# Performance work log

Measured on AMD Instinct MI355X. Metric: run time of the kernel, lower is better.

Reference implementation:

```python
import jax, jax.numpy as jnp
import numpy as np

N_AUTHOR = 100000
N_PAPER = 200000
D = 128          # embedding_dim
E = 600000       # edges (used in both directions: author->paper and paper->author)
S = 100000       # supervision edges
L = 2            # n_layers


def setup_inputs() -> dict:
    key = jax.random.key(0)
    ks = jax.random.split(key, 14)
    s = 1.0 / np.sqrt(D)
    return {
        "x_author": jax.random.normal(ks[0], (N_AUTHOR, D), jnp.float32),
        "x_paper": jax.random.normal(ks[1], (N_PAPER, D), jnp.float32),
        "edge_author": jax.random.randint(ks[2], (E,), 0, N_AUTHOR, jnp.int32),
        "edge_paper": jax.random.randint(ks[3], (E,), 0, N_PAPER, jnp.int32),
        "sup_author": jax.random.randint(ks[4], (S,), 0, N_AUTHOR, jnp.int32),
        "sup_paper": jax.random.randint(ks[5], (S,), 0, N_PAPER, jnp.int32),
        # per-layer stacked Linear params (W is [in, out]; equivalent to torch x @ W.T + b)
        "W_self_author": jax.random.uniform(ks[6], (L, D, D), jnp.float32, -s, s),
        "b_self_author": jax.random.uniform(ks[7], (L, D), jnp.float32, -s, s),
        "W_self_paper": jax.random.uniform(ks[8], (L, D, D), jnp.float32, -s, s),
        "b_self_paper": jax.random.uniform(ks[9], (L, D), jnp.float32, -s, s),
        "W_a2p": jax.random.uniform(ks[10], (L, D, D), jnp.float32, -s, s),  # message_('author','writes','paper')
        "b_a2p": jax.random.uniform(ks[11], (L, D), jnp.float32, -s, s),
        "W_p2a": jax.random.uniform(ks[12], (L, D, D), jnp.float32, -s, s),  # message_('paper','rev_writes','author')
        "b_p2a": jax.random.uniform(ks[13], (L, D), jnp.float32, -s, s),
    }


def reference(x_author, x_paper, edge_author, edge_paper, sup_author, sup_paper,
              W_self_author, b_self_author, W_self_paper, b_self_paper,
              W_a2p, b_a2p, W_p2a, b_p2a):
    n_layers = W_self_author.shape[0]
    n_author = x_author.shape[0]
    n_paper = x_paper.shape[0]
    for l in range(n_layers):
        # gather src features -> per-edge linear -> scatter-sum to dst (aggr='sum')
        msg_to_paper = jax.ops.segment_sum(
            x_author[edge_author] @ W_a2p[l] + b_a2p[l], edge_paper, num_segments=n_paper)
        msg_to_author = jax.ops.segment_sum(
            x_paper[edge_paper] @ W_p2a[l] + b_p2a[l], edge_author, num_segments=n_author)
        # self-loop projection + aggregated incoming messages
        new_author = x_author @ W_self_author[l] + b_self_author[l] + msg_to_author
        new_paper = x_paper @ W_self_paper[l] + b_self_paper[l] + msg_to_paper
        if l < n_layers - 1:  # nonlinearity between layers
            new_author = jax.nn.relu(new_author)
            new_paper = jax.nn.relu(new_paper)
        x_author, x_paper = new_author, new_paper
    # supervision link scores: dot product of paired embeddings
    return (x_author[sup_author] * x_paper[sup_paper]).sum(axis=-1)
```

## Files before the change

kernel.cpp:

```cpp
#include <hip/hip_runtime.h>
#include <stdint.h>

#define D 128
#define SCAN_TILE 1024
#define CB_SHIFT 11
#define CB_NODES 2048
#define CHE 2048

typedef __attribute__((ext_vector_type(8))) short bf16x8_t;
typedef __attribute__((ext_vector_type(4))) float f32x4_t;

__device__ inline unsigned short f2bf(float x) {
    unsigned int u = __float_as_uint(x);
    unsigned int r = (u + 0x7fffu + ((u >> 16) & 1u)) >> 16;
    return (unsigned short)r;
}
__device__ inline float bflo(unsigned v) { return __uint_as_float(v << 16); }
__device__ inline float bfhi(unsigned v) { return __uint_as_float(v & 0xffff0000u); }

__global__ __launch_bounds__(256) void f32_to_bf16_duo(
        const float* __restrict__ inA, unsigned short* __restrict__ outA, int n8A,
        const float* __restrict__ inP, unsigned short* __restrict__ outP, int n8P) {
    int stride = gridDim.x * blockDim.x;
    int total = n8A + n8P;
    for (int i = blockIdx.x * blockDim.x + threadIdx.x; i < total; i += stride) {
        const float* in; unsigned short* out; int j;
        if (i < n8A) { in = inA; out = outA; j = i; }
        else         { in = inP; out = outP; j = i - n8A; }
        float4 v0 = *(const float4*)(in + (size_t)j * 8);
        float4 v1 = *(const float4*)(in + (size_t)j * 8 + 4);
        uint4 o;
        o.x = f2bf(v0.x) | ((unsigned)f2bf(v0.y) << 16);
        o.y = f2bf(v0.z) | ((unsigned)f2bf(v0.w) << 16);
        o.z = f2bf(v1.x) | ((unsigned)f2bf(v1.y) << 16);
        o.w = f2bf(v1.z) | ((unsigned)f2bf(v1.w) << 16);
        *(uint4*)(out + (size_t)j * 8) = o;
    }
}

__global__ void count_deg_kernel(const int* __restrict__ ea, const int* __restrict__ ep,
                                 int E, int* __restrict__ degA, int* __restrict__ degP) {
    int stride = gridDim.x * blockDim.x;
    for (int e = blockIdx.x * blockDim.x + threadIdx.x; e < E; e += stride) {
        atomicAdd(&degA[ea[e]], 1);
        atomicAdd(&degP[ep[e]], 1);
    }
}

__global__ __launch_bounds__(256) void scan_partials_kernel(
        const int* __restrict__ degA, int nA,
        const int* __restrict__ degP, int nP, int gA,
        int* __restrict__ partials) {
    const int* deg; int n;
    int b = blockIdx.x;
    if (b < gA) { deg = degA; n = nA; }
    else        { deg = degP; n = nP; b -= gA; }
    int tid = threadIdx.x;
    int i0 = b * SCAN_TILE + tid * 4;
    int s = 0;
    if (i0 + 3 < n) {
        int4 d = *(const int4*)(deg + i0);
        s = d.x + d.y + d.z + d.w;
    } else {
        for (int j = 0; j < 4; ++j) if (i0 + j < n) s += deg[i0 + j];
    }
#pragma unroll
    for (int off = 32; off; off >>= 1) s += __shfl_xor(s, off);
    __shared__ int wsum[4];
    if ((tid & 63) == 0) wsum[tid >> 6] = s;
    __syncthreads();
    if (tid == 0) partials[blockIdx.x] = wsum[0] + wsum[1] + wsum[2] + wsum[3];
}

__global__ __launch_bounds__(1024) void scan_block_sums_kernel(
        int* __restrict__ partials, int gA, int gP,
        int* __restrict__ rsA_end, int* __restrict__ rsP_end) {
    __shared__ int s[1024];
    int n = gA + gP;
    int tid = threadIdx.x;
    int v = (tid < n) ? partials[tid] : 0;
    s[tid] = v;
    __syncthreads();
    for (int off = 1; off < 1024; off <<= 1) {
        int add = 0;
        if (tid >= off && ((tid < gA) || (tid - off >= gA))) add = s[tid - off];
        __syncthreads();
        s[tid] += add;
        __syncthreads();
    }
    if (tid == gA - 1)  *rsA_end = s[tid];
    if (tid == n - 1)   *rsP_end = s[tid];
    if (tid < n) partials[tid] = s[tid] - v;
}

__global__ __launch_bounds__(256) void scan_write_kernel(
        const int* __restrict__ degA, int nA, int* __restrict__ rsA,
        const int* __restrict__ degP, int nP, int* __restrict__ rsP,
        int gA, const int* __restrict__ partials) {
    const int* deg; int n; int* rs;
    int b = blockIdx.x;
    int part = partials[blockIdx.x];
    if (b < gA) { deg = degA; n = nA; rs = rsA; }
    else        { deg = degP; n = nP; rs = rsP; b -= gA; }
    int tid = threadIdx.x;
    int lane = tid & 63, wid = tid >> 6;
    int i0 = b * SCAN_TILE + tid * 4;

    int4 d = make_int4(0, 0, 0, 0);
    if (i0 + 3 < n) {
        d = *(const int4*)(deg + i0);
    } else {
        if (i0 + 0 < n) d.x = deg[i0 + 0];
        if (i0 + 1 < n) d.y = deg[i0 + 1];
        if (i0 + 2 < n) d.z = deg[i0 + 2];
        if (i0 + 3 < n) d.w = deg[i0 + 3];
    }
    int tsum = d.x + d.y + d.z + d.w;

    int x = tsum;
#pragma unroll
    for (int off = 1; off < 64; off <<= 1) {
        int y = __shfl_up(x, off);
        if (lane >= off) x += y;
    }
    int excl = x - tsum;

    __shared__ int wsum[4];
    if (lane == 63) wsum[wid] = x;
    __syncthreads();
    int woff = 0;
#pragma unroll
    for (int w = 0; w < 4; ++w) if (w < wid) woff += wsum[w];

    int off0 = part + woff + excl;
    int4 o;
    o.x = off0;
    o.y = off0 + d.x;
    o.z = o.y + d.y;
    o.w = o.z + d.z;
    if (i0 + 3 < n) {
        *(int4*)(rs + i0) = o;
    } else {
        if (i0 + 0 < n) rs[i0 + 0] = o.x;
        if (i0 + 1 < n) rs[i0 + 1] = o.y;
        if (i0 + 2 < n) rs[i0 + 2] = o.z;
        if (i0 + 3 < n) rs[i0 + 3] = o.w;
    }
}

__global__ __launch_bounds__(256) void gcur_init_kernel(
        const int* __restrict__ rsA, int nbcA,
        const int* __restrict__ rsP, int nbc, int E, int* __restrict__ gcur) {
    int i = blockIdx.x * blockDim.x + threadIdx.x;
    if (i < nbcA)                gcur[i] = rsA[i << CB_SHIFT];
    else if (i < nbc)            gcur[i] = E + rsP[(i - nbcA) << CB_SHIFT];
}

__global__ __launch_bounds__(256) void multisplit_kernel(
        const int* __restrict__ ea, const int* __restrict__ ep, int E,
        int nbcA, int* __restrict__ gcur, unsigned* __restrict__ buf) {
    __shared__ int hist[256];
    __shared__ int off[256];
    __shared__ int cnt2[256];
    __shared__ int gbase[256];
    __shared__ unsigned cbuf[2 * CHE];
    __shared__ unsigned char bkt[2 * CHE];

    int tid = threadIdx.x;
    int e0 = blockIdx.x * CHE;
    int ecnt = E - e0; if (ecnt > CHE) ecnt = CHE;

    hist[tid] = 0;
    __syncthreads();

    for (int k = tid; k < ecnt; k += 256) {
        int a = ea[e0 + k], p = ep[e0 + k];
        atomicAdd(&hist[a >> CB_SHIFT], 1);
        atomicAdd(&hist[nbcA + (p >> CB_SHIFT)], 1);
    }
    __syncthreads();

    int v = hist[tid];
    off[tid] = v;
    __syncthreads();
    for (int o = 1; o < 256; o <<= 1) {
        int y = (tid >= o) ? off[tid - o] : 0;
        __syncthreads();
        off[tid] += y;
        __syncthreads();
    }
    int excl = off[tid] - v;
    off[tid] = excl;
    cnt2[tid] = 0;
    if (v > 0) gbase[tid] = atomicAdd(&gcur[tid], v);
    __syncthreads();

    for (int k = tid; k < ecnt; k += 256) {
        int a = ea[e0 + k], p = ep[e0 + k];
        int bA = a >> CB_SHIFT;
        int iA = off[bA] + atomicAdd(&cnt2[bA], 1);
        cbuf[iA] = ((unsigned)p << CB_SHIFT) | (unsigned)(a & (CB_NODES - 1));
        bkt[iA] = (unsigned char)bA;
        int bP = nbcA + (p >> CB_SHIFT);
        int iP = off[bP] + atomicAdd(&cnt2[bP], 1);
        cbuf[iP] = ((unsigned)a << CB_SHIFT) | (unsigned)(p & (CB_NODES - 1));
        bkt[iP] = (unsigned char)bP;
    }
    __syncthreads();

    int total = 2 * ecnt;
    for (int i = tid; i < total; i += 256) {
        int b = bkt[i];
        buf[(size_t)gbase[b] + (i - off[b])] = cbuf[i];
    }
}

__global__ __launch_bounds__(1024) void fine_csr_kernel(
        const int* __restrict__ rsA, int nA, int nbcA, int* __restrict__ csrA,
        const int* __restrict__ rsP, int nP, int* __restrict__ csrP,
        const unsigned* __restrict__ buf, int E) {
    __shared__ int base[CB_NODES + 1];
    __shared__ int cnt[CB_NODES];
    const int* rs; int* csr; int n; int d0; const unsigned* mybuf;
    int b = blockIdx.x;
    if (b < nbcA) { rs = rsA; csr = csrA; n = nA; d0 = b << CB_SHIFT; mybuf = buf; }
    else { rs = rsP; csr = csrP; n = nP; d0 = (b - nbcA) << CB_SHIFT; mybuf = buf + E; }
    int nd = n - d0; if (nd > CB_NODES) nd = CB_NODES;

    int tid = threadIdx.x;
    for (int i = tid; i <= nd; i += 1024) base[i] = rs[d0 + i];
    for (int i = tid; i < nd; i += 1024) cnt[i] = 0;
    __syncthreads();

    int g0 = base[0], g1 = base[nd];
    for (int j = g0 + tid; j < g1; j += 1024) {
        unsigned pk = mybuf[j];
        int li = pk & (CB_NODES - 1);
        int src = (int)(pk >> CB_SHIFT);
        int pos = base[li] + atomicAdd(&cnt[li], 1);
        csr[pos] = src;
    }
}

__global__ __launch_bounds__(256) void pack_w_kernel(
        const float* __restrict__ WsA, const float* __restrict__ WsP,
        const float* __restrict__ Wa2p, const float* __restrict__ Wp2a,
        unsigned short* __restrict__ Bpack) {
    int combo = blockIdx.x >> 4;
    int e = (blockIdx.x & 15) * 256 + threadIdx.x;
    int layer = combo >> 1;
    const float* Ws = ((combo & 1) ? WsP : WsA) + (size_t)layer * D * D;
    const float* Wm = ((combo & 1) ? Wa2p : Wp2a) + (size_t)layer * D * D;

    int f = e >> 6, lane = e & 63;
    int nf = f >> 3, ks = f & 7;
    int k0 = ks * 32 + (lane >> 4) * 8;
    int col = nf * 16 + (lane & 15);

    unsigned short v[8];
#pragma unroll
    for (int j = 0; j < 8; ++j) {
        int k = k0 + j;
        float x = (k < D) ? Ws[(size_t)k * D + col] : Wm[(size_t)(k - D) * D + col];
        v[j] = f2bf(x);
    }
    uint4 o;
    o.x = v[0] | ((unsigned)v[1] << 16);
    o.y = v[2] | ((unsigned)v[3] << 16);
    o.z = v[4] | ((unsigned)v[5] << 16);
    o.w = v[6] | ((unsigned)v[7] << 16);
    *(uint4*)(Bpack + (size_t)combo * 32768 + (size_t)e * 8) = o;
}

__global__ __launch_bounds__(256) void aggregate_duo(
        const unsigned short* __restrict__ srcA, const int* __restrict__ rsA,
        const int* __restrict__ csrA, int nA, unsigned short* __restrict__ aggA,
        const unsigned short* __restrict__ srcP, const int* __restrict__ rsP,
        const int* __restrict__ csrP, int nP, unsigned short* __restrict__ aggP) {
    int gw   = (blockIdx.x * 256 + threadIdx.x) >> 6;
    int lane = threadIdx.x & 63;
    int sub  = lane >> 4;
    int sl   = lane & 15;

    const unsigned short* xsrc; const int* rs; const int* csr;
    unsigned short* agg; int d;
    if (gw < nA) { d = gw;      xsrc = srcA; rs = rsA; csr = csrA; agg = aggA; }
    else {
        d = gw - nA;
        if (d >= nP) return;
        xsrc = srcP; rs = rsP; csr = csrP; agg = aggP;
    }

    int s0 = rs[d], s1 = rs[d + 1];
    float acc[8] = {0.f, 0.f, 0.f, 0.f, 0.f, 0.f, 0.f, 0.f};
    for (int j = s0 + sub; j < s1; j += 4) {
        int s = csr[j];
        uint4 v = *(const uint4*)(xsrc + (size_t)s * D + sl * 8);
        acc[0] += bflo(v.x); acc[1] += bfhi(v.x);
        acc[2] += bflo(v.y); acc[3] += bfhi(v.y);
        acc[4] += bflo(v.z); acc[5] += bfhi(v.z);
        acc[6] += bflo(v.w); acc[7] += bfhi(v.w);
    }
#pragma unroll
    for (int i = 0; i < 8; ++i) {
        acc[i] += __shfl_xor(acc[i], 16);
        acc[i] += __shfl_xor(acc[i], 32);
    }
    if (sub == 0) {
        uint4 o;
        o.x = f2bf(acc[0]) | ((unsigned)f2bf(acc[1]) << 16);
        o.y = f2bf(acc[2]) | ((unsigned)f2bf(acc[3]) << 16);
        o.z = f2bf(acc[4]) | ((unsigned)f2bf(acc[5]) << 16);
        o.w = f2bf(acc[6]) | ((unsigned)f2bf(acc[7]) << 16);
        *(uint4*)(agg + (size_t)d * D + sl * 8) = o;
    }
}

__global__ __launch_bounds__(256) void linear_mfma_duo(
        const unsigned short* __restrict__ xsA, const unsigned short* __restrict__ xmA,
        const unsigned short* __restrict__ BpA, const float* __restrict__ bsA,
        const float* __restrict__ bmA, const int* __restrict__ degA_, int nA,
        unsigned short* __restrict__ outA, int gmA,
        const unsigned short* __restrict__ xsP, const unsigned short* __restrict__ xmP,
        const unsigned short* __restrict__ BpP, const float* __restrict__ bsP,
        const float* __restrict__ bmP, const int* __restrict__ degP_, int nP,
        unsigned short* __restrict__ outP, int relu) {
    __shared__ uint4 lds4[2048];
    unsigned char* lds = (unsigned char*)lds4;
    int tid = threadIdx.x;
    int wave = tid >> 6, lane = tid & 63;

    const unsigned short *xs, *xm, *Bpack; const float *bs, *bm;
    const int* deg; int n; unsigned short* out;
    int b = blockIdx.x;
    if (b < gmA) { xs = xsA; xm = xmA; Bpack = BpA; bs = bsA; bm = bmA;
                   deg = degA_; n = nA; out = outA; }
    else { b -= gmA; xs = xsP; xm = xmP; Bpack = BpP; bs = bsP; bm = bmP;
           deg = degP_; n = nP; out = outP; }
    int r_base = b * 64;

    const bf16x8_t* bp = (const bf16x8_t*)Bpack;
    bf16x8_t bb[2][8];
#pragma unroll
    for (int nf2 = 0; nf2 < 2; ++nf2)
#pragma unroll
        for (int ks = 0; ks < 8; ++ks)
            bb[nf2][ks] = bp[((wave * 2 + nf2) * 8 + ks) * 64 + lane];

#pragma unroll
    for (int i = 0; i < 8; ++i) {
        int c = i * 256 + tid;
        int row = c >> 5;
        int kc = (c & 31) * 8;
        int rg = r_base + row;
        uint4 w = make_uint4(0, 0, 0, 0);
        if (rg < n) {
            const unsigned short* src = (kc < D) ? (xs + (size_t)rg * D + kc)
                                                 : (xm + (size_t)rg * D + (kc - D));
            w = *(const uint4*)src;
        }
        unsigned addr = ((unsigned)(row * 512 + kc * 2)) ^ ((unsigned)((row & 7) << 4));
        *(uint4*)(lds + addr) = w;
    }
    __syncthreads();

    f32x4_t acc[4][2];
#pragma unroll
    for (int rt = 0; rt < 4; ++rt)
#pragma unroll
        for (int nf2 = 0; nf2 < 2; ++nf2) acc[rt][nf2] = (f32x4_t){0.f, 0.f, 0.f, 0.f};

#pragma unroll
    for (int rt = 0; rt < 4; ++rt) {
        int lrow = rt * 16 + (lane & 15);
        bf16x8_t a[8];
#pragma unroll
        for (int ks = 0; ks < 8; ++ks) {
            unsigned addr = ((unsigned)(lrow * 512 + ks * 64 + (lane >> 4) * 16))
                            ^ ((unsigned)((lrow & 7) << 4));
            a[ks] = *(const bf16x8_t*)(lds + addr);
        }
#pragma unroll
        for (int ks = 0; ks < 8; ++ks) {
            acc[rt][0] = __builtin_amdgcn_mfma_f32_16x16x32_bf16(a[ks], bb[0][ks], acc[rt][0], 0, 0, 0);
            acc[rt][1] = __builtin_amdgcn_mfma_f32_16x16x32_bf16(a[ks], bb[1][ks], acc[rt][1], 0, 0, 0);
        }
    }

#pragma unroll
    for (int nf2 = 0; nf2 < 2; ++nf2) {
        int col = wave * 32 + nf2 * 16 + (lane & 15);
        float bsv = bs[col], bmv = bm[col];
#pragma unroll
        for (int rt = 0; rt < 4; ++rt) {
            int rb2 = r_base + rt * 16 + (lane >> 4) * 4;
#pragma unroll
            for (int rr = 0; rr < 4; ++rr) {
                int r = rb2 + rr;
                if (r < n) {
                    float dgv = (float)deg[r];
                    float v = acc[rt][nf2][rr] + bsv + dgv * bmv;
                    if (relu) v = fmaxf(v, 0.f);
                    out[(size_t)r * D + col] = f2bf(v);
                }
            }
        }
    }
}

__global__ __launch_bounds__(256) void dot_kernel(
        const unsigned short* __restrict__ za, const unsigned short* __restrict__ zp,
        const int* __restrict__ sa, const int* __restrict__ sp, int S,
        float* __restrict__ out) {
    int gw   = (blockIdx.x * 256 + threadIdx.x) >> 6;
    int lane = threadIdx.x & 63;
    int nw   = (gridDim.x * 256) >> 6;
    for (int i = gw; i < S; i += nw) {
        int a = sa[i], p = sp[i];
        unsigned ua = *(const unsigned*)(za + (size_t)a * D + lane * 2);
        unsigned up = *(const unsigned*)(zp + (size_t)p * D + lane * 2);
        float s = bflo(ua) * bflo(up) + bfhi(ua) * bfhi(up);
#pragma unroll
        for (int off = 32; off > 0; off >>= 1) s += __shfl_xor(s, off);
        if (lane == 0) out[i] = s;
    }
}

extern "C" void kernel_launch(void* const* d_in, const int* in_sizes, int n_in,
                              void* d_out, int out_size, void* d_ws, size_t ws_size,
                              hipStream_t stream) {
    const float* x_a  = (const float*)d_in[0];
    const float* x_p  = (const float*)d_in[1];
    const int*   ea   = (const int*)d_in[2];
    const int*   ep   = (const int*)d_in[3];
    const int*   sa   = (const int*)d_in[4];
    const int*   sp   = (const int*)d_in[5];
    const float* WsA  = (const float*)d_in[6];
    const float* bsA  = (const float*)d_in[7];
    const float* WsP  = (const float*)d_in[8];
    const float* bsP  = (const float*)d_in[9];
    const float* Wa2p = (const float*)d_in[10];
    const float* ba2p = (const float*)d_in[11];
    const float* Wp2a = (const float*)d_in[12];
    const float* bp2a = (const float*)d_in[13];

    const int nA = in_sizes[0] / D;
    const int nP = in_sizes[1] / D;
    const int E  = in_sizes[2];
    const int S  = in_sizes[4];

    char* ws = (char*)d_ws;
    size_t curoff = 0;
    auto alloc = [&](size_t bytes) -> void* {
        void* p = ws + curoff;
        curoff = (curoff + bytes + 255) & ~(size_t)255;
        return p;
    };
    unsigned short* xb_a  = (unsigned short*)alloc((size_t)nA * D * 2);
    unsigned short* xb_p  = (unsigned short*)alloc((size_t)nP * D * 2);
    unsigned short* agg_a = (unsigned short*)alloc((size_t)nA * D * 2);
    unsigned short* agg_p = (unsigned short*)alloc((size_t)nP * D * 2);
    unsigned short* y_a   = (unsigned short*)alloc((size_t)nA * D * 2);
    unsigned short* y_p   = (unsigned short*)alloc((size_t)nP * D * 2);
    unsigned short* z_a   = (unsigned short*)alloc((size_t)nA * D * 2);
    unsigned short* z_p   = (unsigned short*)alloc((size_t)nP * D * 2);
    int* degA = (int*)alloc((size_t)nA * 4);
    int* degP = (int*)alloc((size_t)nP * 4);
    int* rsA  = (int*)alloc(((size_t)nA + 1) * 4);
    int* rsP  = (int*)alloc(((size_t)nP + 1) * 4);
    int* csrA = (int*)alloc((size_t)E * 4);
    int* csrP = (int*)alloc((size_t)E * 4);
    const int gA = (nA + SCAN_TILE - 1) / SCAN_TILE;
    const int gP = (nP + SCAN_TILE - 1) / SCAN_TILE;
    int* partials = (int*)alloc((size_t)(gA + gP) * 4);
    unsigned short* Bpack = (unsigned short*)alloc((size_t)4 * 32768 * 2);

    const int nbcA = (nA + CB_NODES - 1) >> CB_SHIFT;
    const int nbcP = (nP + CB_NODES - 1) >> CB_SHIFT;
    const int NBC  = nbcA + nbcP;
    unsigned* buf = (unsigned*)z_a;
    int* gcur = (int*)z_p;

    f32_to_bf16_duo<<<3072, 256, 0, stream>>>(x_a, xb_a, nA * D / 8,
                                              x_p, xb_p, nP * D / 8);
    size_t deg_bytes = (size_t)((char*)degP - (char*)degA) + (size_t)nP * 4;
    hipMemsetAsync(degA, 0, deg_bytes, stream);
    pack_w_kernel<<<64, 256, 0, stream>>>(WsA, WsP, Wa2p, Wp2a, Bpack);
    count_deg_kernel<<<1024, 256, 0, stream>>>(ea, ep, E, degA, degP);
    scan_partials_kernel<<<gA + gP, 256, 0, stream>>>(degA, nA, degP, nP, gA, partials);
    scan_block_sums_kernel<<<1, 1024, 0, stream>>>(partials, gA, gP, rsA + nA, rsP + nP);
    scan_write_kernel<<<gA + gP, 256, 0, stream>>>(degA, nA, rsA,
                                                   degP, nP, rsP, gA, partials);
    gcur_init_kernel<<<1, 256, 0, stream>>>(rsA, nbcA, rsP, NBC, E, gcur);
    multisplit_kernel<<<(E + CHE - 1) / CHE, 256, 0, stream>>>(ea, ep, E, nbcA, gcur, buf);
    fine_csr_kernel<<<NBC, 1024, 0, stream>>>(rsA, nA, nbcA, csrA,
                                              rsP, nP, csrP, buf, E);

    const int gmA = (nA + 63) / 64;
    const int gmP = (nP + 63) / 64;
    const int gAgg = (nA + nP + 3) / 4;

    aggregate_duo<<<gAgg, 256, 0, stream>>>(xb_p, rsA, csrA, nA, agg_a,
                                            xb_a, rsP, csrP, nP, agg_p);
    linear_mfma_duo<<<gmA + gmP, 256, 0, stream>>>(
        xb_a, agg_a, Bpack + 0 * 32768, bsA, bp2a, degA, nA, y_a, gmA,
        xb_p, agg_p, Bpack + 1 * 32768, bsP, ba2p, degP, nP, y_p, 1);

    aggregate_duo<<<gAgg, 256, 0, stream>>>(y_p, rsA, csrA, nA, agg_a,
                                            y_a, rsP, csrP, nP, agg_p);
    linear_mfma_duo<<<gmA + gmP, 256, 0, stream>>>(
        y_a, agg_a, Bpack + 2 * 32768, bsA + D, bp2a + D, degA, nA, z_a, gmA,
        y_p, agg_p, Bpack + 3 * 32768, bsP + D, ba2p + D, degP, nP, z_p, 0);

    dot_kernel<<<(S + 3) / 4, 256, 0, stream>>>(z_a, z_p, sa, sp, S, (float*)d_out);
}
```

Measured before the change: 478.9 us.

## Build CSR via coarse histogram instead of per-node degree count and scan

Replaces the per-node atomic degree count and three-kernel global scan with a coarse bucket histogram plus a single small scan. The fine CSR kernel now derives per-node degrees and row starts locally in shared memory from each bucket's edges. Bucket size drops to 1024 nodes so one 1024-thread block covers a bucket, and the multisplit kernel moves to 512 threads. It also drops a mask from the bf16 high-half extraction in aggregation, which adds a tiny low-bit error in exchange for one fewer instruction per element.

```diff
diff --git a/kernel.cpp b/kernel.cpp
--- a/kernel.cpp
+++ b/kernel.cpp
@@ -2,10 +2,10 @@
 #include <stdint.h>
 
 #define D 128
-#define SCAN_TILE 1024
-#define CB_SHIFT 11
-#define CB_NODES 2048
+#define CB_SHIFT 10
+#define CB_NODES 1024
 #define CHE 2048
+#define NBC_MAX 512
 
 typedef __attribute__((ext_vector_type(8))) short bf16x8_t;
 typedef __attribute__((ext_vector_type(4))) float f32x4_t;
@@ -16,7 +16,6 @@
     return (unsigned short)r;
 }
 __device__ inline float bflo(unsigned v) { return __uint_as_float(v << 16); }
-__device__ inline float bfhi(unsigned v) { return __uint_as_float(v & 0xffff0000u); }
 
 __global__ __launch_bounds__(256) void f32_to_bf16_duo(
         const float* __restrict__ inA, unsigned short* __restrict__ outA, int n8A,
@@ -38,152 +37,77 @@
     }
 }
 
-__global__ void count_deg_kernel(const int* __restrict__ ea, const int* __restrict__ ep,
-                                 int E, int* __restrict__ degA, int* __restrict__ degP) {
-    int stride = gridDim.x * blockDim.x;
-    for (int e = blockIdx.x * blockDim.x + threadIdx.x; e < E; e += stride) {
-        atomicAdd(&degA[ea[e]], 1);
-        atomicAdd(&degP[ep[e]], 1);
-    }
-}
-
-__global__ __launch_bounds__(256) void scan_partials_kernel(
-        const int* __restrict__ degA, int nA,
-        const int* __restrict__ degP, int nP, int gA,
-        int* __restrict__ partials) {
-    const int* deg; int n;
-    int b = blockIdx.x;
-    if (b < gA) { deg = degA; n = nA; }
-    else        { deg = degP; n = nP; b -= gA; }
+__global__ __launch_bounds__(256) void coarse_count_kernel(
+        const int* __restrict__ ea, const int* __restrict__ ep, int E,
+        int nbcA, int nbc, int* __restrict__ chist) {
+    __shared__ int hist[NBC_MAX];
     int tid = threadIdx.x;
-    int i0 = b * SCAN_TILE + tid * 4;
-    int s = 0;
-    if (i0 + 3 < n) {
-        int4 d = *(const int4*)(deg + i0);
-        s = d.x + d.y + d.z + d.w;
-    } else {
-        for (int j = 0; j < 4; ++j) if (i0 + j < n) s += deg[i0 + j];
-    }
-#pragma unroll
-    for (int off = 32; off; off >>= 1) s += __shfl_xor(s, off);
-    __shared__ int wsum[4];
-    if ((tid & 63) == 0) wsum[tid >> 6] = s;
-    __syncthreads();
-    if (tid == 0) partials[blockIdx.x] = wsum[0] + wsum[1] + wsum[2] + wsum[3];
-}
-
-__global__ __launch_bounds__(1024) void scan_block_sums_kernel(
-        int* __restrict__ partials, int gA, int gP,
-        int* __restrict__ rsA_end, int* __restrict__ rsP_end) {
-    __shared__ int s[1024];
-    int n = gA + gP;
-    int tid = threadIdx.x;
-    int v = (tid < n) ? partials[tid] : 0;
-    s[tid] = v;
-    __syncthreads();
-    for (int off = 1; off < 1024; off <<= 1) {
-        int add = 0;
-        if (tid >= off && ((tid < gA) || (tid - off >= gA))) add = s[tid - off];
-        __syncthreads();
-        s[tid] += add;
-        __syncthreads();
-    }
-    if (tid == gA - 1)  *rsA_end = s[tid];
-    if (tid == n - 1)   *rsP_end = s[tid];
-    if (tid < n) partials[tid] = s[tid] - v;
-}
-
-__global__ __launch_bounds__(256) void scan_write_kernel(
-        const int* __restrict__ degA, int nA, int* __restrict__ rsA,
-        const int* __restrict__ degP, int nP, int* __restrict__ rsP,
-        int gA, const int* __restrict__ partials) {
-    const int* deg; int n; int* rs;
-    int b = blockIdx.x;
-    int part = partials[blockIdx.x];
-    if (b < gA) { deg = degA; n = nA; rs = rsA; }
-    else        { deg = degP; n = nP; rs = rsP; b -= gA; }
-    int tid = threadIdx.x;
-    int lane = tid & 63, wid = tid >> 6;
-    int i0 = b * SCAN_TILE + tid * 4;
-
-    int4 d = make_int4(0, 0, 0, 0);
-    if (i0 + 3 < n) {
-        d = *(const int4*)(deg + i0);
-    } else {
-        if (i0 + 0 < n) d.x = deg[i0 + 0];
-        if (i0 + 1 < n) d.y = deg[i0 + 1];
-        if (i0 + 2 < n) d.z = deg[i0 + 2];
-        if (i0 + 3 < n) d.w = deg[i0 + 3];
-    }
-    int tsum = d.x + d.y + d.z + d.w;
-
-    int x = tsum;
-#pragma unroll
-    for (int off = 1; off < 64; off <<= 1) {
-        int y = __shfl_up(x, off);
-        if (lane >= off) x += y;
-    }
-    int excl = x - tsum;
-
-    __shared__ int wsum[4];
-    if (lane == 63) wsum[wid] = x;
-    __syncthreads();
-    int woff = 0;
-#pragma unroll
-    for (int w = 0; w < 4; ++w) if (w < wid) woff += wsum[w];
-
-    int off0 = part + woff + excl;
-    int4 o;
-    o.x = off0;
-    o.y = off0 + d.x;
-    o.z = o.y + d.y;
-    o.w = o.z + d.z;
-    if (i0 + 3 < n) {
-        *(int4*)(rs + i0) = o;
-    } else {
-        if (i0 + 0 < n) rs[i0 + 0] = o.x;
-        if (i0 + 1 < n) rs[i0 + 1] = o.y;
-        if (i0 + 2 < n) rs[i0 + 2] = o.z;
-        if (i0 + 3 < n) rs[i0 + 3] = o.w;
-    }
-}
-
-__global__ __launch_bounds__(256) void gcur_init_kernel(
-        const int* __restrict__ rsA, int nbcA,
-        const int* __restrict__ rsP, int nbc, int E, int* __restrict__ gcur) {
-    int i = blockIdx.x * blockDim.x + threadIdx.x;
-    if (i < nbcA)                gcur[i] = rsA[i << CB_SHIFT];
-    else if (i < nbc)            gcur[i] = E + rsP[(i - nbcA) << CB_SHIFT];
-}
-
-__global__ __launch_bounds__(256) void multisplit_kernel(
-        const int* __restrict__ ea, const int* __restrict__ ep, int E,
-        int nbcA, int* __restrict__ gcur, unsigned* __restrict__ buf) {
-    __shared__ int hist[256];
-    __shared__ int off[256];
-    __shared__ int cnt2[256];
-    __shared__ int gbase[256];
-    __shared__ unsigned cbuf[2 * CHE];
-    __shared__ unsigned char bkt[2 * CHE];
-
-    int tid = threadIdx.x;
+    for (int i = tid; i < NBC_MAX; i += 256) hist[i] = 0;
+    __syncthreads();
     int e0 = blockIdx.x * CHE;
     int ecnt = E - e0; if (ecnt > CHE) ecnt = CHE;
-
-    hist[tid] = 0;
-    __syncthreads();
-
     for (int k = tid; k < ecnt; k += 256) {
         int a = ea[e0 + k], p = ep[e0 + k];
         atomicAdd(&hist[a >> CB_SHIFT], 1);
         atomicAdd(&hist[nbcA + (p >> CB_SHIFT)], 1);
     }
     __syncthreads();
+    for (int i = tid; i < nbc; i += 256)
+        if (hist[i]) atomicAdd(&chist[i], hist[i]);
+}
+
+__global__ __launch_bounds__(NBC_MAX) void coarse_scan_kernel(
+        const int* __restrict__ chist, int nbcA, int nbc, int E,
+        int* __restrict__ gcur, int* __restrict__ cbase,
+        int* __restrict__ rsA_end, int* __restrict__ rsP_end) {
+    __shared__ int s[NBC_MAX];
+    int tid = threadIdx.x;
+    int v = (tid < nbc) ? chist[tid] : 0;
+    s[tid] = v;
+    __syncthreads();
+    for (int off = 1; off < NBC_MAX; off <<= 1) {
+        int add = 0;
+        if (tid >= off && ((tid < nbcA) || (tid - off >= nbcA))) add = s[tid - off];
+        __syncthreads();
+        s[tid] += add;
+        __syncthreads();
+    }
+    int excl = s[tid] - v;
+    if (tid < nbc) {
+        cbase[tid] = excl;
+        gcur[tid] = (tid < nbcA) ? excl : E + excl;
+    }
+    if (tid == 0) { *rsA_end = E; *rsP_end = E; }
+}
+
+__global__ __launch_bounds__(512) void multisplit_kernel(
+        const int* __restrict__ ea, const int* __restrict__ ep, int E,
+        int nbcA, int* __restrict__ gcur, unsigned* __restrict__ buf) {
+    __shared__ int hist[NBC_MAX];
+    __shared__ int off[NBC_MAX];
+    __shared__ int cnt2[NBC_MAX];
+    __shared__ int gbase[NBC_MAX];
+    __shared__ unsigned cbuf[2 * CHE];
+    __shared__ unsigned short bkt[2 * CHE];
+
+    int tid = threadIdx.x;
+    int e0 = blockIdx.x * CHE;
+    int ecnt = E - e0; if (ecnt > CHE) ecnt = CHE;
+
+    hist[tid] = 0;
+    __syncthreads();
+
+    for (int k = tid; k < ecnt; k += 512) {
+        int a = ea[e0 + k], p = ep[e0 + k];
+        atomicAdd(&hist[a >> CB_SHIFT], 1);
+        atomicAdd(&hist[nbcA + (p >> CB_SHIFT)], 1);
+    }
+    __syncthreads();
 
     int v = hist[tid];
     off[tid] = v;
     __syncthreads();
-    for (int o = 1; o < 256; o <<= 1) {
+    for (int o = 1; o < NBC_MAX; o <<= 1) {
         int y = (tid >= o) ? off[tid - o] : 0;
         __syncthreads();
         off[tid] += y;
@@ -195,50 +119,75 @@
     if (v > 0) gbase[tid] = atomicAdd(&gcur[tid], v);
     __syncthreads();
 
-    for (int k = tid; k < ecnt; k += 256) {
+    for (int k = tid; k < ecnt; k += 512) {
         int a = ea[e0 + k], p = ep[e0 + k];
         int bA = a >> CB_SHIFT;
         int iA = off[bA] + atomicAdd(&cnt2[bA], 1);
         cbuf[iA] = ((unsigned)p << CB_SHIFT) | (unsigned)(a & (CB_NODES - 1));
-        bkt[iA] = (unsigned char)bA;
+        bkt[iA] = (unsigned short)bA;
         int bP = nbcA + (p >> CB_SHIFT);
         int iP = off[bP] + atomicAdd(&cnt2[bP], 1);
         cbuf[iP] = ((unsigned)a << CB_SHIFT) | (unsigned)(p & (CB_NODES - 1));
-        bkt[iP] = (unsigned char)bP;
+        bkt[iP] = (unsigned short)bP;
     }
     __syncthreads();
 
     int total = 2 * ecnt;
-    for (int i = tid; i < total; i += 256) {
+    for (int i = tid; i < total; i += 512) {
         int b = bkt[i];
         buf[(size_t)gbase[b] + (i - off[b])] = cbuf[i];
     }
 }
 
 __global__ __launch_bounds__(1024) void fine_csr_kernel(
-        const int* __restrict__ rsA, int nA, int nbcA, int* __restrict__ csrA,
-        const int* __restrict__ rsP, int nP, int* __restrict__ csrP,
-        const unsigned* __restrict__ buf, int E) {
-    __shared__ int base[CB_NODES + 1];
+        const unsigned* __restrict__ buf, int E, int nbcA,
+        const int* __restrict__ cbase, const int* __restrict__ chist,
+        int* __restrict__ rsA, int* __restrict__ degA, int* __restrict__ csrA, int nA,
+        int* __restrict__ rsP, int* __restrict__ degP, int* __restrict__ csrP, int nP) {
     __shared__ int cnt[CB_NODES];
-    const int* rs; int* csr; int n; int d0; const unsigned* mybuf;
+    __shared__ int s[CB_NODES];
+    __shared__ int pos[CB_NODES];
     int b = blockIdx.x;
-    if (b < nbcA) { rs = rsA; csr = csrA; n = nA; d0 = b << CB_SHIFT; mybuf = buf; }
-    else { rs = rsP; csr = csrP; n = nP; d0 = (b - nbcA) << CB_SHIFT; mybuf = buf + E; }
-    int nd = n - d0; if (nd > CB_NODES) nd = CB_NODES;
-
     int tid = threadIdx.x;
-    for (int i = tid; i <= nd; i += 1024) base[i] = rs[d0 + i];
-    for (int i = tid; i < nd; i += 1024) cnt[i] = 0;
-    __syncthreads();
-
-    int g0 = base[0], g1 = base[nd];
-    for (int j = g0 + tid; j < g1; j += 1024) {
-        unsigned pk = mybuf[j];
+    int isA = (b < nbcA);
+    int d0 = (isA ? b : b - nbcA) << CB_SHIFT;
+    int n  = isA ? nA : nP;
+    int* rs  = isA ? rsA  : rsP;
+    int* deg = isA ? degA : degP;
+    int* csr = isA ? csrA : csrP;
+    int cb   = cbase[b];
+    int cntE = chist[b];
+    size_t bstart = (isA ? (size_t)0 : (size_t)E) + (size_t)cb;
+
+    cnt[tid] = 0;
+    __syncthreads();
+    for (int j = tid; j < cntE; j += 1024)
+        atomicAdd(&cnt[buf[bstart + j] & (CB_NODES - 1)], 1);
+    __syncthreads();
+
+    int v = cnt[tid];
+    s[tid] = v;
+    __syncthreads();
+    for (int o = 1; o < CB_NODES; o <<= 1) {
+        int y = (tid >= o) ? s[tid - o] : 0;
+        __syncthreads();
+        s[tid] += y;
+        __syncthreads();
+    }
+    int excl = s[tid] - v;
+    int d = d0 + tid;
+    if (d < n) { rs[d] = cb + excl; deg[d] = v; }
+
+    pos[tid] = 0;
+    cnt[tid] = excl;
+    __syncthreads();
+
+    for (int j = tid; j < cntE; j += 1024) {
+        unsigned pk = buf[bstart + j];
         int li = pk & (CB_NODES - 1);
         int src = (int)(pk >> CB_SHIFT);
-        int pos = base[li] + atomicAdd(&cnt[li], 1);
-        csr[pos] = src;
+        int p = cb + cnt[li] + atomicAdd(&pos[li], 1);
+        csr[p] = src;
     }
 }
 
@@ -296,10 +245,10 @@
     for (int j = s0 + sub; j < s1; j += 4) {
         int s = csr[j];
         uint4 v = *(const uint4*)(xsrc + (size_t)s * D + sl * 8);
-        acc[0] += bflo(v.x); acc[1] += bfhi(v.x);
-        acc[2] += bflo(v.y); acc[3] += bfhi(v.y);
-        acc[4] += bflo(v.z); acc[5] += bfhi(v.z);
-        acc[6] += bflo(v.w); acc[7] += bfhi(v.w);
+        acc[0] += bflo(v.x); acc[1] += __uint_as_float(v.x);
+        acc[2] += bflo(v.y); acc[3] += __uint_as_float(v.y);
+        acc[4] += bflo(v.z); acc[5] += __uint_as_float(v.z);
+        acc[6] += bflo(v.w); acc[7] += __uint_as_float(v.w);
     }
 #pragma unroll
     for (int i = 0; i < 8; ++i) {
@@ -419,7 +368,8 @@
         int a = sa[i], p = sp[i];
         unsigned ua = *(const unsigned*)(za + (size_t)a * D + lane * 2);
         unsigned up = *(const unsigned*)(zp + (size_t)p * D + lane * 2);
-        float s = bflo(ua) * bflo(up) + bfhi(ua) * bfhi(up);
+        float s = bflo(ua) * bflo(up)
+                + __uint_as_float(ua & 0xffff0000u) * __uint_as_float(up & 0xffff0000u);
 #pragma unroll
         for (int off = 32; off > 0; off >>= 1) s += __shfl_xor(s, off);
         if (lane == 0) out[i] = s;
@@ -470,31 +420,29 @@
     int* rsP  = (int*)alloc(((size_t)nP + 1) * 4);
     int* csrA = (int*)alloc((size_t)E * 4);
     int* csrP = (int*)alloc((size_t)E * 4);
-    const int gA = (nA + SCAN_TILE - 1) / SCAN_TILE;
-    const int gP = (nP + SCAN_TILE - 1) / SCAN_TILE;
-    int* partials = (int*)alloc((size_t)(gA + gP) * 4);
     unsigned short* Bpack = (unsigned short*)alloc((size_t)4 * 32768 * 2);
 
     const int nbcA = (nA + CB_NODES - 1) >> CB_SHIFT;
     const int nbcP = (nP + CB_NODES - 1) >> CB_SHIFT;
     const int NBC  = nbcA + nbcP;
     unsigned* buf = (unsigned*)z_a;
-    int* gcur = (int*)z_p;
+    int* gcur  = (int*)z_p;
+    int* cbase = gcur + NBC_MAX;
+    int* chist = cbase + NBC_MAX;
+
+    const int nchunk = (E + CHE - 1) / CHE;
 
     f32_to_bf16_duo<<<3072, 256, 0, stream>>>(x_a, xb_a, nA * D / 8,
                                               x_p, xb_p, nP * D / 8);
-    size_t deg_bytes = (size_t)((char*)degP - (char*)degA) + (size_t)nP * 4;
-    hipMemsetAsync(degA, 0, deg_bytes, stream);
+    hipMemsetAsync(chist, 0, NBC_MAX * 4, stream);
     pack_w_kernel<<<64, 256, 0, stream>>>(WsA, WsP, Wa2p, Wp2a, Bpack);
-    count_deg_kernel<<<1024, 256, 0, stream>>>(ea, ep, E, degA, degP);
-    scan_partials_kernel<<<gA + gP, 256, 0, stream>>>(degA, nA, degP, nP, gA, partials);
-    scan_block_sums_kernel<<<1, 1024, 0, stream>>>(partials, gA, gP, rsA + nA, rsP + nP);
-    scan_write_kernel<<<gA + gP, 256, 0, stream>>>(degA, nA, rsA,
-                                                   degP, nP, rsP, gA, partials);
-    gcur_init_kernel<<<1, 256, 0, stream>>>(rsA, nbcA, rsP, NBC, E, gcur);
-    multisplit_kernel<<<(E + CHE - 1) / CHE, 256, 0, stream>>>(ea, ep, E, nbcA, gcur, buf);
-    fine_csr_kernel<<<NBC, 1024, 0, stream>>>(rsA, nA, nbcA, csrA,
-                                              rsP, nP, csrP, buf, E);
+    coarse_count_kernel<<<nchunk, 256, 0, stream>>>(ea, ep, E, nbcA, NBC, chist);
+    coarse_scan_kernel<<<1, NBC_MAX, 0, stream>>>(chist, nbcA, NBC, E,
+                                                  gcur, cbase, rsA + nA, rsP + nP);
+    multisplit_kernel<<<nchunk, 512, 0, stream>>>(ea, ep, E, nbcA, gcur, buf);
+    fine_csr_kernel<<<NBC, 1024, 0, stream>>>(buf, E, nbcA, cbase, chist,
+                                              rsA, degA, csrA, nA,
+                                              rsP, degP, csrP, nP);
 
     const int gmA = (nA + 63) / 64;
     const int gmP = (nP + 63) / 64;
```

Result: faster. 432.0 us (-9.8%).
